# Kernel tuning notes

Hardware: AMD Instinct MI355X
Metric: run time of the kernel (lower is better)

## Reference

```python
import jax, jax.numpy as jnp
import numpy as np

B, N, C_IN, H_GNN, H_RNN = 8, 4096, 32, 64, 64
NFEAT = C_IN + H_RNN          # 96
NOUT = 4 * H_RNN              # 256


def setup_inputs() -> dict:
    key = jax.random.key(0)
    ks = jax.random.split(key, 10)
    stdv1 = 1.0 / np.sqrt(H_GNN)
    stdv2 = 1.0 / np.sqrt(NOUT)
    return {
        "input_tensor": jax.random.normal(ks[0], (B, N, C_IN), jnp.float32),
        "h_cur": jax.random.normal(ks[1], (B, N, H_RNN), jnp.float32),
        "c_cur": jax.random.normal(ks[2], (B, N, H_RNN), jnp.float32),
        "adj": jax.random.uniform(ks[3], (N, N), jnp.float32),
        # GCN layer 1 params (nfeat -> nhid)
        "W1": jax.random.uniform(ks[4], (NFEAT, H_GNN), jnp.float32, -stdv1, stdv1),
        "mask1": jnp.ones((N, N), jnp.float32),
        "b1": jax.random.uniform(ks[5], (H_GNN,), jnp.float32, -stdv1, stdv1),
        # GCN layer 2 params (nhid -> 4*rnn_hidden)
        "W2": jax.random.uniform(ks[6], (H_GNN, NOUT), jnp.float32, -stdv2, stdv2),
        "mask2": jnp.ones((N, N), jnp.float32),
        "b2": jax.random.uniform(ks[7], (NOUT,), jnp.float32, -stdv2, stdv2),
    }


def _gcn_layer(x, adj, mask, W, b):
    # support = x @ W : [B,N,d]; output = (adj*mask) @ support : [B,N,d]
    support = jnp.einsum("bnc,cd->bnd", x, W)
    return jnp.einsum("mn,bnd->bmd", adj * mask, support) + b


def reference(input_tensor, h_cur, c_cur, adj, W1, mask1, b1, W2, mask2, b2):
    combined = jnp.concatenate([input_tensor, h_cur], axis=-1)  # [B,N,C+H]
    x1 = jax.nn.relu(_gcn_layer(combined, adj, mask1, W1, b1))  # [B,N,H_GNN]
    cc = _gcn_layer(x1, adj, mask2, W2, b2)                      # [B,N,4H]
    cc_i, cc_f, cc_o, cc_g = jnp.split(cc, 4, axis=-1)
    i = jax.nn.sigmoid(cc_i)
    f = jax.nn.sigmoid(cc_f)
    o = jax.nn.sigmoid(cc_o)
    g = jnp.tanh(cc_g)
    c_next = f * c_cur + i * g
    h_next = o * jnp.tanh(c_next)
    return (h_next, c_next)
```

## Files before the change

kernel.cpp:

```cpp
#include <hip/hip_runtime.h>
#include <hip/hip_bf16.h>
#include <hip/hip_fp16.h>
#include <stdint.h>

typedef _Float16 half_t;
typedef _Float16 half8 __attribute__((ext_vector_type(8)));
typedef float f32x4 __attribute__((ext_vector_type(4)));

#define NN 4096
#define OFF_W1THI  0u
#define OFF_W1TLO  16384u
#define OFF_S1HI   32768u
#define OFF_S1LO   (32768u + 4194304u)
#define OFF_XP0    (32768u + 2u*4194304u)
#define OFF_XP1    (OFF_XP0 + 8388608u)

__device__ __forceinline__ float sigmoidf_(float x) { return 1.f / (1.f + __expf(-x)); }
__device__ __forceinline__ float tanhf_(float x)    { return 1.f - 2.f / (__expf(2.f * x) + 1.f); }

__global__ void prep_w1t(const float* __restrict__ w1,
                         half_t* __restrict__ whi, half_t* __restrict__ wlo) {
    int i = blockIdx.x * 256 + threadIdx.x;
    if (i >= 96 * 64) return;
    int c = i >> 6, d = i & 63;
    float v = w1[i];
    half_t h = (half_t)v;
    whi[d * 96 + c] = h;
    wlo[d * 96 + c] = (half_t)(v - (float)h);
}

__global__ __launch_bounds__(256) void k1_gemm(
    const float* __restrict__ inp, const float* __restrict__ hcur,
    const half_t* __restrict__ wthi, const half_t* __restrict__ wtlo,
    half_t* __restrict__ s1hi, half_t* __restrict__ s1lo)
{
    __shared__ half_t Ch[64 * 96], Cl[64 * 96], Wh[64 * 96], Wl[64 * 96];
    const int t = threadIdx.x;
    const int l = t & 63, w = t >> 6, lr = l & 15, lg = l >> 4;
    const int b = blockIdx.x >> 6;
    const int kb = blockIdx.x & 63;
    const int nBase = kb * 64;

    {
        const uint32_t* sh = (const uint32_t*)wthi;
        const uint32_t* sl = (const uint32_t*)wtlo;
        uint32_t* dh = (uint32_t*)Wh;
        uint32_t* dl = (uint32_t*)Wl;
        for (int i = t; i < 3072; i += 256) { dh[i] = sh[i]; dl[i] = sl[i]; }
    }
#pragma unroll
    for (int i = 0; i < 6; ++i) {
        int f4 = t + i * 256;
        int row = f4 / 24, slot = f4 % 24;
        int n = nBase + row;
        f32x4 v; int c0;
        if (slot < 8) { c0 = slot * 4; v = *(const f32x4*)(inp + ((size_t)b * NN + n) * 32 + c0); }
        else { c0 = 32 + (slot - 8) * 4; v = *(const f32x4*)(hcur + ((size_t)b * NN + n) * 64 + (c0 - 32)); }
#pragma unroll
        for (int jj = 0; jj < 4; ++jj) {
            float x = v[jj];
            half_t hh = (half_t)x;
            Ch[row * 96 + c0 + jj] = hh;
            Cl[row * 96 + c0 + jj] = (half_t)(x - (float)hh);
        }
    }
    __syncthreads();

    const f32x4 z = {0.f, 0.f, 0.f, 0.f};
    f32x4 acc[4] = {z, z, z, z};
#pragma unroll
    for (int kk = 0; kk < 3; ++kk) {
        const int qo = (w * 16 + lr) * 96 + kk * 32 + lg * 8;
        half8 cf_h = *(const half8*)(Ch + qo);
        half8 cf_l = *(const half8*)(Cl + qo);
#pragma unroll
        for (int dt = 0; dt < 4; ++dt) {
            const int po = (dt * 16 + lr) * 96 + kk * 32 + lg * 8;
            half8 wf_h = *(const half8*)(Wh + po);
            half8 wf_l = *(const half8*)(Wl + po);
            acc[dt] = __builtin_amdgcn_mfma_f32_16x16x32_f16(wf_h, cf_h, acc[dt], 0, 0, 0);
            acc[dt] = __builtin_amdgcn_mfma_f32_16x16x32_f16(wf_h, cf_l, acc[dt], 0, 0, 0);
            acc[dt] = __builtin_amdgcn_mfma_f32_16x16x32_f16(wf_l, cf_h, acc[dt], 0, 0, 0);
        }
    }
    const int kc = w * 16 + lr;
#pragma unroll
    for (int dt = 0; dt < 4; ++dt)
#pragma unroll
        for (int j4 = 0; j4 < 4; ++j4) {
            int d = dt * 16 + lg * 4 + j4;
            float v = acc[dt][j4];
            half_t hh = (half_t)v;
            size_t o = ((size_t)kb * 512 + b * 64 + d) * 64 + kc;
            s1hi[o] = hh;
            s1lo[o] = (half_t)(v - (float)hh);
        }
}

template<int PASSES>
__global__ __launch_bounds__(1024) void gemm_bn(
    const float* __restrict__ adj, const float* __restrict__ mask,
    const half_t* __restrict__ xhi, const half_t* __restrict__ xlo,
    float* __restrict__ out0, float* __restrict__ out1)
{
    __shared__ half_t Ah[2 * 128 * 64];
    __shared__ half_t Xh[2 * 128 * 64];
    __shared__ half_t Al[PASSES == 3 ? 2 * 128 * 64 : 4];
    __shared__ half_t Xl[PASSES == 3 ? 2 * 128 * 64 : 4];
    const int t = threadIdx.x;
    const int l = t & 63, w = t >> 6, lr = l & 15, lg = l >> 4;
    const int wm = w >> 2, wn = w & 3;
    const int bx = blockIdx.x;
    const int mt_ = bx & 31, ks = (bx >> 5) & 1, nb = bx >> 6;
    const int mBase = mt_ * 128, jBase = nb * 128;
    float* __restrict__ outp = ks ? out1 : out0;

    const f32x4 z = {0.f, 0.f, 0.f, 0.f};
    f32x4 acc[2][2] = {{z, z}, {z, z}};

    const int srow = t >> 3, skc = t & 7;
    const int sbyte = (srow * 128 + skc * 16) ^ ((srow & 7) << 4);

    f32x4 pa0, pa1, pm0, pm1;
    half8 pxh, pxl;

#define ISSUE_LOADS(IT)                                                          \
    {                                                                            \
        const int kb = ks * 32 + (IT);                                           \
        const int k0 = kb * 64;                                                  \
        size_t ga = (size_t)(mBase + srow) * NN + k0 + skc * 8;                  \
        pa0 = *(const f32x4*)(adj + ga);                                         \
        pa1 = *(const f32x4*)(adj + ga + 4);                                     \
        pm0 = *(const f32x4*)(mask + ga);                                        \
        pm1 = *(const f32x4*)(mask + ga + 4);                                    \
        size_t gx = ((size_t)kb * 512 + jBase + srow) * 64 + skc * 8;            \
        pxh = *(const half8*)(xhi + gx);                                         \
        if constexpr (PASSES == 3) pxl = *(const half8*)(xlo + gx);              \
    }

#define CONVERT_WRITE(P)                                                         \
    {                                                                            \
        const int off = (P) * 16384;                                             \
        half8 hv, lv;                                                            \
        _Pragma("unroll")                                                        \
        for (int jj = 0; jj < 4; ++jj) {                                         \
            float p0 = pa0[jj] * pm0[jj];                                        \
            float p1 = pa1[jj] * pm1[jj];                                        \
            half_t h0 = (half_t)p0, h1 = (half_t)p1;                             \
            hv[jj] = h0; hv[jj + 4] = h1;                                        \
            if constexpr (PASSES == 3) {                                         \
                lv[jj] = (half_t)(p0 - (float)h0);                               \
                lv[jj + 4] = (half_t)(p1 - (float)h1);                           \
            }                                                                    \
        }                                                                        \
        *(half8*)((char*)Ah + off + sbyte) = hv;                                 \
        *(half8*)((char*)Xh + off + sbyte) = pxh;                                \
        if constexpr (PASSES == 3) {                                             \
            *(half8*)((char*)Al + off + sbyte) = lv;                             \
            *(half8*)((char*)Xl + off + sbyte) = pxl;                            \
        }                                                                        \
    }

    ISSUE_LOADS(0);
    CONVERT_WRITE(0);
    __syncthreads();

    for (int it = 0; it < 32; ++it) {
        const int p = it & 1;
        const int pofs = p * 16384;
        if (it + 1 < 32) ISSUE_LOADS(it + 1);
        __builtin_amdgcn_sched_barrier(0);
#pragma unroll
        for (int kk = 0; kk < 2; ++kk) {
            half8 fa_h[2], fa_l[2], fx_h[2], fx_l[2];
#pragma unroll
            for (int mt = 0; mt < 2; ++mt) {
                int r = wm * 32 + mt * 16 + lr;
                int byte = ((r * 128 + kk * 64 + lg * 16) ^ ((r & 7) << 4)) + pofs;
                fa_h[mt] = *(const half8*)((const char*)Ah + byte);
                if constexpr (PASSES == 3)
                    fa_l[mt] = *(const half8*)((const char*)Al + byte);
            }
#pragma unroll
            for (int nt = 0; nt < 2; ++nt) {
                int r = wn * 32 + nt * 16 + lr;
                int byte = ((r * 128 + kk * 64 + lg * 16) ^ ((r & 7) << 4)) + pofs;
                fx_h[nt] = *(const half8*)((const char*)Xh + byte);
                if constexpr (PASSES == 3)
                    fx_l[nt] = *(const half8*)((const char*)Xl + byte);
            }
            __builtin_amdgcn_sched_barrier(0);
#pragma unroll
            for (int mt = 0; mt < 2; ++mt)
#pragma unroll
                for (int nt = 0; nt < 2; ++nt) {
                    acc[mt][nt] = __builtin_amdgcn_mfma_f32_16x16x32_f16(fa_h[mt], fx_h[nt], acc[mt][nt], 0, 0, 0);
                    if constexpr (PASSES == 3) {
                        acc[mt][nt] = __builtin_amdgcn_mfma_f32_16x16x32_f16(fa_l[mt], fx_h[nt], acc[mt][nt], 0, 0, 0);
                        acc[mt][nt] = __builtin_amdgcn_mfma_f32_16x16x32_f16(fa_h[mt], fx_l[nt], acc[mt][nt], 0, 0, 0);
                    }
                }
        }
        if (it + 1 < 32) CONVERT_WRITE(p ^ 1);
        __syncthreads();
    }

#pragma unroll
    for (int mt = 0; mt < 2; ++mt)
#pragma unroll
        for (int nt = 0; nt < 2; ++nt) {
            int jcol = jBase + wn * 32 + nt * 16 + lr;
#pragma unroll
            for (int j4 = 0; j4 < 4; ++j4) {
                int mrow = mBase + wm * 32 + mt * 16 + lg * 4 + j4;
                outp[(size_t)mrow * 512 + jcol] = acc[mt][nt][j4];
            }
        }
#undef ISSUE_LOADS
#undef CONVERT_WRITE
}

__global__ __launch_bounds__(256) void k2e(
    const float* __restrict__ p0, const float* __restrict__ p1,
    const float* __restrict__ b1,
    half_t* __restrict__ x1s)
{
    int base = blockIdx.x * 256 + threadIdx.x;
#pragma unroll
    for (int rpt = 0; rpt < 4; ++rpt) {
        int idx4 = base + rpt * 131072;
        int m = idx4 >> 7, jq = idx4 & 127;
        int j0 = jq * 4, d0 = j0 & 63;
        size_t e = (size_t)m * 512 + j0;
        f32x4 v = *(const f32x4*)(p0 + e);
        f32x4 u = *(const f32x4*)(p1 + e);
        f32x4 bb = *(const f32x4*)(b1 + d0);
        size_t obase = ((size_t)(m >> 6) * 512 + j0) * 64 + (m & 63);
#pragma unroll
        for (int jj = 0; jj < 4; ++jj) {
            float x = v[jj] + u[jj] + bb[jj];
            x = fmaxf(x, 0.f);
            x1s[obase + (size_t)jj * 64] = (half_t)x;
        }
    }
}

__global__ __launch_bounds__(256) void k4_final(
    const float* __restrict__ y0, const float* __restrict__ y1,
    const float* __restrict__ w2, const float* __restrict__ b2,
    const float* __restrict__ ccur,
    float* __restrict__ outh, float* __restrict__ outc)
{
    __shared__ float Yt[64 * 64];
    __shared__ float W2s[64 * 256];
    const int t = threadIdx.x;
    const int cb = t & 15, rb = t >> 4;
    const int rowBase = blockIdx.x * 64;
    const int bIdx = rowBase >> 12, mBase = rowBase & 4095;

#pragma unroll
    for (int i = 0; i < 4; ++i) {
        int id4 = t + i * 256;
        int r = id4 >> 4, dc = id4 & 15;
        size_t g = (size_t)(mBase + r) * 512 + bIdx * 64 + dc * 4;
        f32x4 v = *(const f32x4*)(y0 + g);
        f32x4 u = *(const f32x4*)(y1 + g);
#pragma unroll
        for (int jj = 0; jj < 4; ++jj) Yt[(dc * 4 + jj) * 64 + r] = v[jj] + u[jj];
    }
#pragma unroll
    for (int i = 0; i < 16; ++i) {
        int id4 = t + i * 256;
        *(f32x4*)(W2s + id4 * 4) = *(const f32x4*)(w2 + id4 * 4);
    }
    __syncthreads();

    const f32x4 z = {0.f, 0.f, 0.f, 0.f};
    f32x4 accG[4][4];
#pragma unroll
    for (int g = 0; g < 4; ++g)
#pragma unroll
        for (int r8 = 0; r8 < 4; ++r8) accG[g][r8] = z;

    for (int d = 0; d < 64; ++d) {
        f32x4 y4 = *(const f32x4*)(Yt + d * 64 + rb * 4);
#pragma unroll
        for (int g = 0; g < 4; ++g) {
            f32x4 w4 = *(const f32x4*)(W2s + d * 256 + g * 64 + cb * 4);
#pragma unroll
            for (int r8 = 0; r8 < 4; ++r8) accG[g][r8] += w4 * y4[r8];
        }
    }

    float b2i[4], b2f[4], b2o[4], b2g[4];
#pragma unroll
    for (int jj = 0; jj < 4; ++jj) {
        b2i[jj] = b2[0 * 64 + cb * 4 + jj];
        b2f[jj] = b2[1 * 64 + cb * 4 + jj];
        b2o[jj] = b2[2 * 64 + cb * 4 + jj];
        b2g[jj] = b2[3 * 64 + cb * 4 + jj];
    }
#pragma unroll
    for (int r8 = 0; r8 < 4; ++r8) {
        int row = rowBase + rb * 4 + r8;
        f32x4 c4 = *(const f32x4*)(ccur + (size_t)row * 64 + cb * 4);
        f32x4 hv, cv;
#pragma unroll
        for (int jj = 0; jj < 4; ++jj) {
            float ii = sigmoidf_(accG[0][r8][jj] + b2i[jj]);
            float ff = sigmoidf_(accG[1][r8][jj] + b2f[jj]);
            float oo = sigmoidf_(accG[2][r8][jj] + b2o[jj]);
            float gg = tanhf_(accG[3][r8][jj] + b2g[jj]);
            float cn = ff * c4[jj] + ii * gg;
            float hn = oo * tanhf_(cn);
            hv[jj] = hn;
            cv[jj] = cn;
        }
        *(f32x4*)(outh + (size_t)row * 64 + cb * 4) = hv;
        *(f32x4*)(outc + (size_t)row * 64 + cb * 4) = cv;
    }
}

extern "C" void kernel_launch(void* const* d_in, const int* in_sizes, int n_in,
                              void* d_out, int out_size, void* d_ws, size_t ws_size,
                              hipStream_t stream) {
    const float* inp   = (const float*)d_in[0];
    const float* hcur  = (const float*)d_in[1];
    const float* ccur  = (const float*)d_in[2];
    const float* adj   = (const float*)d_in[3];
    const float* w1    = (const float*)d_in[4];
    const float* mask1 = (const float*)d_in[5];
    const float* b1    = (const float*)d_in[6];
    const float* w2    = (const float*)d_in[7];
    const float* mask2 = (const float*)d_in[8];
    const float* b2    = (const float*)d_in[9];

    char* ws = (char*)d_ws;
    half_t* w1thi = (half_t*)(ws + OFF_W1THI);
    half_t* w1tlo = (half_t*)(ws + OFF_W1TLO);
    half_t* s1hi  = (half_t*)(ws + OFF_S1HI);
    half_t* s1lo  = (half_t*)(ws + OFF_S1LO);
    half_t* x1s   = (half_t*)(ws + OFF_S1HI);
    float*  xp0   = (float*)(ws + OFF_XP0);
    float*  xp1   = (float*)(ws + OFF_XP1);
    float*  y0    = (float*)(ws + OFF_XP0);
    float*  y1    = (float*)(ws + OFF_XP1);

    float* hout = (float*)d_out;
    float* cout = hout + (size_t)8 * 4096 * 64;

    prep_w1t<<<24, 256, 0, stream>>>(w1, w1thi, w1tlo);
    k1_gemm<<<512, 256, 0, stream>>>(inp, hcur, w1thi, w1tlo, s1hi, s1lo);
    gemm_bn<3><<<256, 1024, 0, stream>>>(adj, mask1, s1hi, s1lo, xp0, xp1);
    k2e<<<512, 256, 0, stream>>>(xp0, xp1, b1, x1s);
    gemm_bn<1><<<256, 1024, 0, stream>>>(adj, mask2, x1s, x1s, y0, y1);
    k4_final<<<512, 256, 0, stream>>>(y0, y1, w2, b2, ccur, hout, cout);
}
```

Before: 159.5 us.

## Halve GEMM N-tile to 64, use 512-thread blocks, single-buffer LDS

```diff
diff --git a/kernel.cpp b/kernel.cpp
--- a/kernel.cpp
+++ b/kernel.cpp
@@ -98,76 +98,87 @@
 }
 
 template<int PASSES>
-__global__ __launch_bounds__(1024) void gemm_bn(
+__global__ __launch_bounds__(512) void gemm_bn(
     const float* __restrict__ adj, const float* __restrict__ mask,
     const half_t* __restrict__ xhi, const half_t* __restrict__ xlo,
     float* __restrict__ out0, float* __restrict__ out1)
 {
-    __shared__ half_t Ah[2 * 128 * 64];
-    __shared__ half_t Xh[2 * 128 * 64];
-    __shared__ half_t Al[PASSES == 3 ? 2 * 128 * 64 : 4];
-    __shared__ half_t Xl[PASSES == 3 ? 2 * 128 * 64 : 4];
+    __shared__ half_t Ah[128 * 64];
+    __shared__ half_t Al[PASSES == 3 ? 128 * 64 : 4];
+    __shared__ half_t Xh[64 * 64];
+    __shared__ half_t Xl[PASSES == 3 ? 64 * 64 : 4];
     const int t = threadIdx.x;
     const int l = t & 63, w = t >> 6, lr = l & 15, lg = l >> 4;
-    const int wm = w >> 2, wn = w & 3;
+    const int wm = w >> 1, wn = w & 1;
     const int bx = blockIdx.x;
     const int mt_ = bx & 31, ks = (bx >> 5) & 1, nb = bx >> 6;
-    const int mBase = mt_ * 128, jBase = nb * 128;
+    const int mBase = mt_ * 128, jBase = nb * 64;
     float* __restrict__ outp = ks ? out1 : out0;
 
     const f32x4 z = {0.f, 0.f, 0.f, 0.f};
     f32x4 acc[2][2] = {{z, z}, {z, z}};
 
-    const int srow = t >> 3, skc = t & 7;
-    const int sbyte = (srow * 128 + skc * 16) ^ ((srow & 7) << 4);
-
-    f32x4 pa0, pa1, pm0, pm1;
+    const int arow = t >> 2, akc = (t & 3) * 2;
+    const int ab0 = (arow * 128 + akc * 16) ^ ((arow & 7) << 4);
+    const int ab1 = (arow * 128 + (akc + 1) * 16) ^ ((arow & 7) << 4);
+    const int xrow = t >> 3, xkc = t & 7;
+    const int xb = (xrow * 128 + xkc * 16) ^ ((xrow & 7) << 4);
+
+    f32x4 pa0, pa1, pa2, pa3, pm0, pm1, pm2, pm3;
     half8 pxh, pxl;
 
 #define ISSUE_LOADS(IT)                                                          \
     {                                                                            \
         const int kb = ks * 32 + (IT);                                           \
-        const int k0 = kb * 64;                                                  \
-        size_t ga = (size_t)(mBase + srow) * NN + k0 + skc * 8;                  \
+        size_t ga = (size_t)(mBase + arow) * NN + kb * 64 + akc * 8;             \
         pa0 = *(const f32x4*)(adj + ga);                                         \
         pa1 = *(const f32x4*)(adj + ga + 4);                                     \
+        pa2 = *(const f32x4*)(adj + ga + 8);                                     \
+        pa3 = *(const f32x4*)(adj + ga + 12);                                    \
         pm0 = *(const f32x4*)(mask + ga);                                        \
         pm1 = *(const f32x4*)(mask + ga + 4);                                    \
-        size_t gx = ((size_t)kb * 512 + jBase + srow) * 64 + skc * 8;            \
+        pm2 = *(const f32x4*)(mask + ga + 8);                                    \
+        pm3 = *(const f32x4*)(mask + ga + 12);                                   \
+        size_t gx = ((size_t)kb * 512 + jBase + xrow) * 64 + xkc * 8;            \
         pxh = *(const half8*)(xhi + gx);                                         \
         if constexpr (PASSES == 3) pxl = *(const half8*)(xlo + gx);              \
     }
 
-#define CONVERT_WRITE(P)                                                         \
+#define CONVERT_WRITE()                                                          \
     {                                                                            \
-        const int off = (P) * 16384;                                             \
-        half8 hv, lv;                                                            \
+        half8 hv0, lv0, hv1, lv1;                                                \
         _Pragma("unroll")                                                        \
         for (int jj = 0; jj < 4; ++jj) {                                         \
-            float p0 = pa0[jj] * pm0[jj];                                        \
-            float p1 = pa1[jj] * pm1[jj];                                        \
-            half_t h0 = (half_t)p0, h1 = (half_t)p1;                             \
-            hv[jj] = h0; hv[jj + 4] = h1;                                        \
+            float q0 = pa0[jj] * pm0[jj];                                        \
+            float q1 = pa1[jj] * pm1[jj];                                        \
+            float q2 = pa2[jj] * pm2[jj];                                        \
+            float q3 = pa3[jj] * pm3[jj];                                        \
+            half_t h0 = (half_t)q0, h1 = (half_t)q1;                             \
+            half_t h2 = (half_t)q2, h3 = (half_t)q3;                             \
+            hv0[jj] = h0; hv0[jj + 4] = h1;                                      \
+            hv1[jj] = h2; hv1[jj + 4] = h3;                                      \
             if constexpr (PASSES == 3) {                                         \
-                lv[jj] = (half_t)(p0 - (float)h0);                               \
-                lv[jj + 4] = (half_t)(p1 - (float)h1);                           \
+                lv0[jj] = (half_t)(q0 - (float)h0);                              \
+                lv0[jj + 4] = (half_t)(q1 - (float)h1);                          \
+                lv1[jj] = (half_t)(q2 - (float)h2);                              \
+                lv1[jj + 4] = (half_t)(q3 - (float)h3);                          \
             }                                                                    \
         }                                                                        \
-        *(half8*)((char*)Ah + off + sbyte) = hv;                                 \
-        *(half8*)((char*)Xh + off + sbyte) = pxh;                                \
+        *(half8*)((char*)Ah + ab0) = hv0;                                        \
+        *(half8*)((char*)Ah + ab1) = hv1;                                        \
+        *(half8*)((char*)Xh + xb) = pxh;                                         \
         if constexpr (PASSES == 3) {                                             \
-            *(half8*)((char*)Al + off + sbyte) = lv;                             \
-            *(half8*)((char*)Xl + off + sbyte) = pxl;                            \
+            *(half8*)((char*)Al + ab0) = lv0;                                    \
+            *(half8*)((char*)Al + ab1) = lv1;                                    \
+            *(half8*)((char*)Xl + xb) = pxl;                                     \
         }                                                                        \
     }
 
     ISSUE_LOADS(0);
-    CONVERT_WRITE(0);
-    __syncthreads();
 
     for (int it = 0; it < 32; ++it) {
-        const int p = it & 1;
-        const int pofs = p * 16384;
+        CONVERT_WRITE();
+        __syncthreads();
         if (it + 1 < 32) ISSUE_LOADS(it + 1);
         __builtin_amdgcn_sched_barrier(0);
 #pragma unroll
@@ -176,7 +187,7 @@
 #pragma unroll
             for (int mt = 0; mt < 2; ++mt) {
                 int r = wm * 32 + mt * 16 + lr;
-                int byte = ((r * 128 + kk * 64 + lg * 16) ^ ((r & 7) << 4)) + pofs;
+                int byte = (r * 128 + kk * 64 + lg * 16) ^ ((r & 7) << 4);
                 fa_h[mt] = *(const half8*)((const char*)Ah + byte);
                 if constexpr (PASSES == 3)
                     fa_l[mt] = *(const half8*)((const char*)Al + byte);
@@ -184,7 +195,7 @@
 #pragma unroll
             for (int nt = 0; nt < 2; ++nt) {
                 int r = wn * 32 + nt * 16 + lr;
-                int byte = ((r * 128 + kk * 64 + lg * 16) ^ ((r & 7) << 4)) + pofs;
+                int byte = (r * 128 + kk * 64 + lg * 16) ^ ((r & 7) << 4);
                 fx_h[nt] = *(const half8*)((const char*)Xh + byte);
                 if constexpr (PASSES == 3)
                     fx_l[nt] = *(const half8*)((const char*)Xl + byte);
@@ -201,7 +212,6 @@
                     }
                 }
         }
-        if (it + 1 < 32) CONVERT_WRITE(p ^ 1);
         __syncthreads();
     }
 
@@ -351,8 +361,8 @@
 
     prep_w1t<<<24, 256, 0, stream>>>(w1, w1thi, w1tlo);
     k1_gemm<<<512, 256, 0, stream>>>(inp, hcur, w1thi, w1tlo, s1hi, s1lo);
-    gemm_bn<3><<<256, 1024, 0, stream>>>(adj, mask1, s1hi, s1lo, xp0, xp1);
+    gemm_bn<3><<<512, 512, 0, stream>>>(adj, mask1, s1hi, s1lo, xp0, xp1);
     k2e<<<512, 256, 0, stream>>>(xp0, xp1, b1, x1s);
-    gemm_bn<1><<<256, 1024, 0, stream>>>(adj, mask2, x1s, x1s, y0, y1);
+    gemm_bn<1><<<512, 512, 0, stream>>>(adj, mask2, x1s, x1s, y0, y1);
     k4_final<<<512, 256, 0, stream>>>(y0, y1, w2, b2, ccur, hout, cout);
 }
```

After: 216.9 us. 36.0% more time.
